# Kernel optimization log

Hardware: AMD Instinct MI355X
Metric: run time of the kernel (lower is better)

Reference implementation:

```python
import jax, jax.numpy as jnp
import numpy as np

# SSD-style extra-layer channel pyramid for sample_duration=16 (reconstructed):
CH = [(2048, 512, 1024), (1024, 256, 512), (512, 128, 256)]
DN = ('NCDHW', 'OIDHW', 'NCDHW')
B = 128


def conv3d(x, w, stride=(1, 1, 1), padding='VALID', rhs_dilation=None):
    return jax.lax.conv_general_dilated(
        x, w, window_strides=stride, padding=padding,
        rhs_dilation=rhs_dilation, dimension_numbers=DN)


def setup_inputs() -> dict:
    key = jax.random.key(0)
    ks = iter(jax.random.split(key, 32))
    s = 0.02
    d = {}
    d['x'] = jax.random.normal(next(ks), (B, 2048, 16, 2, 2), jnp.float32)
    d['start_boundaries'] = jax.random.randint(next(ks), (B,), 0, 1000, dtype=jnp.int32)
    # head 0 operates on the backbone feature map directly, kernel (2,2,2)
    d['loc_w0'] = s * jax.random.normal(next(ks), (2, 2048, 2, 2, 2), jnp.float32)
    d['conf_w0'] = s * jax.random.normal(next(ks), (3, 2048, 2, 2, 2), jnp.float32)
    for i, (cin, mid, cout) in enumerate(CH):
        d[f'e{i}_w1'] = s * jax.random.normal(next(ks), (mid, cin, 1, 1, 1), jnp.float32)
        d[f'e{i}_w2'] = s * jax.random.normal(next(ks), (cout, mid, 3, 3, 3), jnp.float32)
        d[f'loc_w{i+1}'] = s * jax.random.normal(next(ks), (2, cout, 2, 2, 2), jnp.float32)
        d[f'conf_w{i+1}'] = s * jax.random.normal(next(ks), (3, cout, 2, 2, 2), jnp.float32)
    return d


def reference(x, start_boundaries, loc_w0, conf_w0,
              e0_w1, e0_w2, loc_w1, conf_w1,
              e1_w1, e1_w2, loc_w2, conf_w2,
              e2_w1, e2_w2, loc_w3, conf_w3):
    del start_boundaries  # only used in test phase
    b = x.shape[0]
    loc_ws = [loc_w0, loc_w1, loc_w2, loc_w3]
    conf_ws = [conf_w0, conf_w1, conf_w2, conf_w3]
    extra = [(e0_w1, e0_w2), (e1_w1, e1_w2), (e2_w1, e2_w2)]
    locs = [conv3d(x, loc_ws[0]).reshape(b, -1)]
    confs = [conv3d(x, conf_ws[0]).reshape(b, -1)]
    h = x
    for i, (w1, w2) in enumerate(extra):
        h = conv3d(h, w1)  # 1x1x1 channel reduce
        # 3x3x3, temporal dilation/stride/padding 2 -> T halves, H/W preserved
        h = conv3d(h, w2, stride=(2, 1, 1),
                   padding=[(2, 2), (1, 1), (1, 1)], rhs_dilation=(2, 1, 1))
        locs.append(conv3d(h, loc_ws[i + 1]).reshape(b, -1))
        confs.append(conv3d(h, conf_ws[i + 1]).reshape(b, -1))
    loc = jnp.concatenate(locs, axis=1).reshape(b, -1, 2)    # [B, 26, 2]
    conf = jnp.concatenate(confs, axis=1).reshape(b, -1, 3)  # [B, 26, 3]
    return (loc, conf)
```

## Files before the change

kernel.cpp:

```cpp
#include <hip/hip_runtime.h>

typedef __bf16 bf16;
typedef bf16 bf16x2 __attribute__((ext_vector_type(2)));
typedef bf16 bf16x8 __attribute__((ext_vector_type(8)));
typedef float f32x4 __attribute__((ext_vector_type(4)));

__device__ __forceinline__ void gload16(const bf16* g, bf16* l) {
  __builtin_amdgcn_global_load_lds((const __attribute__((address_space(1))) void*)g,
                                   (__attribute__((address_space(3))) void*)l, 16, 0, 0);
}

template <bool FULL>
__global__ __launch_bounds__(256) void pack_x(const float* __restrict__ x, bf16* __restrict__ dstbuf) {
  __shared__ float tile[64 * 65];
  const int b = blockIdx.x, cb = blockIdx.y;
  const int t = threadIdx.x;
  const float* src = x + ((size_t)b * 2048 + cb * 64) * 64;
  #pragma unroll
  for (int p = 0; p < 16; ++p) {
    int idx = t + p * 256;
    tile[(idx >> 6) * 65 + (idx & 63)] = src[idx];
  }
  __syncthreads();
  if constexpr (FULL) {
    bf16* dst = dstbuf + (size_t)b * 131072 + cb * 64;
    #pragma unroll
    for (int p = 0; p < 8; ++p) {
      int idx = t + p * 256;
      int dhw = idx >> 5;
      int cl2 = (idx & 31) * 2;
      bf16x2 v;
      v.x = (bf16)tile[cl2 * 65 + dhw];
      v.y = (bf16)tile[(cl2 + 1) * 65 + dhw];
      *(bf16x2*)(dst + (size_t)dhw * 2048 + cl2) = v;
    }
  } else {
    bf16* dst = dstbuf + ((size_t)b * 32) * 2048 + cb * 64;
    const int cl2 = (t & 31) * 2, mr0 = t >> 5;
    #pragma unroll
    for (int p = 0; p < 4; ++p) {
      int mrow = mr0 + p * 8;
      int dd = mrow >> 2, hw = mrow & 3;
      int sdhw = dd * 8 + hw;
      bf16x2 v;
      v.x = (bf16)tile[cl2 * 65 + sdhw];
      v.y = (bf16)tile[(cl2 + 1) * 65 + sdhw];
      *(bf16x2*)(dst + (size_t)mrow * 2048 + cl2) = v;
    }
  }
}

__global__ __launch_bounds__(256) void pack_w0(const float* __restrict__ lw0,
                                               const float* __restrict__ cw0,
                                               bf16* __restrict__ Bh) {
  int idx = blockIdx.x * 256 + threadIdx.x;
  int n = idx >> 13, k = idx & 8191;
  int hw = k >> 11, c = k & 2047;
  float v = 0.f;
  if (n < 10) {
    int kd = n / 5, j = n % 5;
    const float* w = (j < 2) ? (lw0 + j * 16384) : (cw0 + (j - 2) * 16384);
    v = w[c * 8 + kd * 4 + hw];
  }
  Bh[idx] = (bf16)v;
}

__global__ __launch_bounds__(256) void head0_gemm(const bf16* __restrict__ xcl,
                                                  const bf16* __restrict__ Bh,
                                                  float* __restrict__ P) {
  __shared__ bf16 ldsA[64 * 64];
  __shared__ bf16 ldsB[16 * 64];
  const int bm = blockIdx.x, ks = blockIdx.y;
  const int tid = threadIdx.x;
  const int wv = tid >> 6, lane = tid & 63, r = lane & 15, g = lane >> 4;
  f32x4 acc = {0.f, 0.f, 0.f, 0.f};
  for (int k0 = 0; k0 < 1024; k0 += 64) {
    #pragma unroll
    for (int q = 0; q < 2; ++q) {
      int idx = tid + q * 256;
      int row = idx >> 3, cg = idx & 7;
      gload16(xcl + (size_t)(bm * 64 + row) * 8192 + ks * 1024 + k0 + (cg ^ (row & 7)) * 8,
              ldsA + idx * 8);
    }
    if (tid < 128) {
      int row = tid >> 3, cg = tid & 7;
      gload16(Bh + (size_t)row * 8192 + ks * 1024 + k0 + (cg ^ (row & 7)) * 8,
              ldsB + tid * 8);
    }
    __syncthreads();
    #pragma unroll
    for (int ks2 = 0; ks2 < 2; ++ks2) {
      int rowa = wv * 16 + r;
      bf16x8 af = *(const bf16x8*)(ldsA + rowa * 64 + ((ks2 * 4 + g) ^ (rowa & 7)) * 8);
      bf16x8 bf_ = *(const bf16x8*)(ldsB + r * 64 + ((ks2 * 4 + g) ^ (r & 7)) * 8);
      acc = __builtin_amdgcn_mfma_f32_16x16x32_bf16(af, bf_, acc, 0, 0, 0);
    }
    __syncthreads();
  }
  const int m = bm * 64 + wv * 16 + g * 4;
  #pragma unroll
  for (int jr = 0; jr < 4; ++jr)
    P[(size_t)(ks * 2048 + m + jr) * 16 + r] = acc[jr];
}

__global__ __launch_bounds__(128) void head0_combine(const float* __restrict__ P,
                                                     float* __restrict__ out) {
  const int b = blockIdx.x, t = threadIdx.x;
  if (t < 75) {
    int j = t / 15, d = t % 15;
    float s = 0.f;
    #pragma unroll
    for (int ks = 0; ks < 8; ++ks) {
      const float* pb = P + (size_t)(ks * 2048 + b * 16) * 16;
      s += pb[d * 16 + j] + pb[(d + 1) * 16 + 5 + j];
    }
    if (j < 2) out[b * 52 + j * 15 + d] = s;
    else       out[6656 + b * 78 + (j - 2) * 15 + d] = s;
  }
}

__global__ __launch_bounds__(256) void cvt_w1(const float* __restrict__ in, bf16* __restrict__ out, int n8) {
  int i = blockIdx.x * 256 + threadIdx.x;
  if (i < n8) {
    const float4* p = (const float4*)(in + (size_t)i * 8);
    float4 a = p[0], b = p[1];
    bf16x8 v = {(bf16)a.x, (bf16)a.y, (bf16)a.z, (bf16)a.w,
                (bf16)b.x, (bf16)b.y, (bf16)b.z, (bf16)b.w};
    *(bf16x8*)(out + (size_t)i * 8) = v;
  }
}

__global__ __launch_bounds__(256) void pack_w2(const float* __restrict__ w2, bf16* __restrict__ w2p,
                                               int oBase, int cin) {
  __shared__ float tile[64 * 27];
  const int orel = blockIdx.x, cb = blockIdx.y;
  const int o = oBase + orel;
  const float* src = w2 + ((size_t)o * cin + cb * 64) * 27;
  const int t = threadIdx.x;
  for (int idx = t; idx < 1728; idx += 256) tile[idx] = src[idx];
  __syncthreads();
  bf16* dst = w2p + (size_t)orel * 27 * cin + cb * 64;
  for (int idx = t; idx < 1728; idx += 256) {
    int tap = idx >> 6, cl = idx & 63;
    dst[(size_t)tap * cin + cl] = (bf16)tile[cl * 27 + tap];
  }
}

struct GP {
  const bf16* A; const bf16* B; bf16* O;
  int K;
  int ashb, asB, am1, as1, am2, as2;
  int oshb, osB, om1, os1, om2, os2, oOff;
  int lgCv, coutS, oCol0, lgCin;
};

template <int FM, int FN, bool W2M>
__global__ __launch_bounds__(256) void gemm_bf(GP p) {
  constexpr int BM = FM * 32, BN = FN * 32;
  __shared__ bf16 lds[(BM + BN) * 64];
  bf16* ldsA = lds;
  bf16* ldsB = lds + BM * 64;
  const int tid = threadIdx.x;
  const int bm = blockIdx.x, bn = blockIdx.y;

  int aBase[BM / 32], aL[BM / 32];
  #pragma unroll
  for (int q = 0; q < BM / 32; ++q) {
    int idx = tid + q * 256;
    int row = idx >> 3, cg = idx & 7;
    int m = bm * BM + row;
    aBase[q] = (m >> p.ashb) * p.asB + ((m >> 2) & p.am1) * p.as1 + (m & p.am2) * p.as2;
    aL[q] = ((cg ^ row) & 7) * 8;
  }
  int opk[BN / 32];
  int bN[BN / 32], bL[BN / 32];
  int khkw0 = 0, khkw1 = 0, khkw2 = 0, khkw3 = 0;
  #pragma unroll
  for (int q = 0; q < BN / 32; ++q) {
    int idx = tid + q * 256;
    int row = idx >> 3, cg = idx & 7;
    int n = bn * BN + row;
    int sw = ((cg ^ row) & 7) * 8;
    if constexpr (W2M) {
      int op = n & ((1 << p.lgCv) - 1);
      opk[q] = (op * 27 << p.lgCin) + sw;
      bN[q] = 0; bL[q] = 0;
    } else {
      bN[q] = n; bL[q] = sw; opk[q] = 0;
    }
  }
  if constexpr (W2M) {
    const int hwp = (bn * BN) >> p.lgCv;
    const int hp = hwp >> 1, wp = hwp & 1;
    khkw0 = ((1 - hp) * 3 + (1 - wp)) << p.lgCin;
    khkw1 = ((1 - hp) * 3 + (2 - wp)) << p.lgCin;
    khkw2 = ((2 - hp) * 3 + (1 - wp)) << p.lgCin;
    khkw3 = ((2 - hp) * 3 + (2 - wp)) << p.lgCin;
  }

  const int wv = tid >> 6, wm = wv >> 1, wn = wv & 1;
  const int lane = tid & 63, r = lane & 15, g = lane >> 4;

  f32x4 acc[FM][FN];
  const f32x4 zz = {0.f, 0.f, 0.f, 0.f};
  #pragma unroll
  for (int i = 0; i < FM; ++i)
    #pragma unroll
    for (int j = 0; j < FN; ++j) acc[i][j] = zz;

  for (int k0 = 0; k0 < p.K; k0 += 64) {
    #pragma unroll
    for (int q = 0; q < BM / 32; ++q) {
      int idx = tid + q * 256;
      gload16(p.A + aBase[q] + k0 + aL[q], ldsA + idx * 8);
    }
    if constexpr (W2M) {
      const int kd = k0 >> (p.lgCin + 2);
      const int hwsel = (k0 >> p.lgCin) & 3;
      const int c0 = k0 & ((1 << p.lgCin) - 1);
      int kk = (hwsel & 2) ? ((hwsel & 1) ? khkw3 : khkw2)
                           : ((hwsel & 1) ? khkw1 : khkw0);
      const int koff = (kd * 9 << p.lgCin) + kk + c0;
      #pragma unroll
      for (int q = 0; q < BN / 32; ++q) {
        int idx = tid + q * 256;
        gload16(p.B + opk[q] + koff, ldsB + idx * 8);
      }
    } else {
      #pragma unroll
      for (int q = 0; q < BN / 32; ++q) {
        int idx = tid + q * 256;
        gload16(p.B + (size_t)bN[q] * p.K + k0 + bL[q], ldsB + idx * 8);
      }
    }
    __syncthreads();
    #pragma unroll
    for (int ks = 0; ks < 2; ++ks) {
      bf16x8 af[FM], bfr[FN];
      #pragma unroll
      for (int i = 0; i < FM; ++i) {
        int row = wm * FM * 16 + i * 16 + r;
        int pcg = (ks * 4 + g) ^ (row & 7);
        af[i] = *(const bf16x8*)(ldsA + row * 64 + pcg * 8);
      }
      #pragma unroll
      for (int j = 0; j < FN; ++j) {
        int row = wn * FN * 16 + j * 16 + r;
        int pcg = (ks * 4 + g) ^ (row & 7);
        bfr[j] = *(const bf16x8*)(ldsB + row * 64 + pcg * 8);
      }
      #pragma unroll
      for (int i = 0; i < FM; ++i)
        #pragma unroll
        for (int j = 0; j < FN; ++j)
          acc[i][j] = __builtin_amdgcn_mfma_f32_16x16x32_bf16(af[i], bfr[j], acc[i][j], 0, 0, 0);
    }
    __syncthreads();
  }

  #pragma unroll
  for (int i = 0; i < FM; ++i) {
    #pragma unroll
    for (int j = 0; j < FN; ++j) {
      int ncol = bn * BN + wn * FN * 16 + j * 16 + r;
      int outcol = (ncol >> p.lgCv) * p.coutS + p.oCol0 + (ncol & ((1 << p.lgCv) - 1));
      #pragma unroll
      for (int jr = 0; jr < 4; ++jr) {
        int m = bm * BM + wm * FM * 16 + i * 16 + g * 4 + jr;
        int oa = (m >> p.oshb) * p.osB + ((m >> 2) & p.om1) * p.os1 + (m & p.om2) * p.os2 + p.oOff + outcol;
        p.O[oa] = (bf16)acc[i][j][jr];
      }
    }
  }
}

__global__ __launch_bounds__(256) void gemm2_sk64(const bf16* __restrict__ A,
                                                  const bf16* __restrict__ B,
                                                  float* __restrict__ Hf) {
  __shared__ bf16 lds[8192];
  bf16* ldsA = lds;
  bf16* ldsB = lds + 4096;
  const int tid = threadIdx.x;
  const int bm = blockIdx.x, bn = blockIdx.y, z = blockIdx.z;

  int aOff[2], bOff[2];
  #pragma unroll
  for (int q = 0; q < 2; ++q) {
    int idx = tid + q * 256;
    int row = idx >> 3, cg = idx & 7;
    int sw = ((cg ^ row) & 7) * 8;
    int m = bm * 64 + row;
    aOff[q] = (m >> 3) * 20480 + (m & 7) * 2048 + sw;
    int n = bn * 64 + row;
    bOff[q] = (n & 1023) * 13824 + sw;
  }
  const int hwp = (bn * 64) >> 10;
  const int hp = hwp >> 1, wp = hwp & 1;
  const int kk0 = ((1 - hp) * 3 + (1 - wp)) << 9;
  const int kk1 = ((1 - hp) * 3 + (2 - wp)) << 9;
  const int kk2 = ((2 - hp) * 3 + (1 - wp)) << 9;
  const int kk3 = ((2 - hp) * 3 + (2 - wp)) << 9;

  const int wv = tid >> 6, wm = wv >> 1, wn = wv & 1;
  const int lane = tid & 63, r = lane & 15, g = lane >> 4;

  f32x4 acc[2][2];
  const f32x4 zz = {0.f, 0.f, 0.f, 0.f};
  #pragma unroll
  for (int i = 0; i < 2; ++i)
    #pragma unroll
    for (int j = 0; j < 2; ++j) acc[i][j] = zz;

  const int kbeg = z * 3072, kend = kbeg + 3072;
  for (int k0 = kbeg; k0 < kend; k0 += 64) {
    int kd = k0 >> 11, hws = (k0 >> 9) & 3, c0 = k0 & 511;
    int kk = (hws & 2) ? ((hws & 1) ? kk3 : kk2) : ((hws & 1) ? kk1 : kk0);
    int koff = kd * 4608 + kk + c0;
    #pragma unroll
    for (int q = 0; q < 2; ++q) {
      int idx = tid + q * 256;
      gload16(A + aOff[q] + k0, ldsA + idx * 8);
      gload16(B + bOff[q] + koff, ldsB + idx * 8);
    }
    __syncthreads();
    #pragma unroll
    for (int ks = 0; ks < 2; ++ks) {
      bf16x8 af[2], bfr[2];
      #pragma unroll
      for (int i = 0; i < 2; ++i) {
        int row = wm * 32 + i * 16 + r;
        int pcg = (ks * 4 + g) ^ (row & 7);
        af[i] = *(const bf16x8*)(ldsA + row * 64 + pcg * 8);
      }
      #pragma unroll
      for (int j = 0; j < 2; ++j) {
        int row = wn * 32 + j * 16 + r;
        int pcg = (ks * 4 + g) ^ (row & 7);
        bfr[j] = *(const bf16x8*)(ldsB + row * 64 + pcg * 8);
      }
      #pragma unroll
      for (int i = 0; i < 2; ++i)
        #pragma unroll
        for (int j = 0; j < 2; ++j)
          acc[i][j] = __builtin_amdgcn_mfma_f32_16x16x32_bf16(af[i], bfr[j], acc[i][j], 0, 0, 0);
    }
    __syncthreads();
  }

  #pragma unroll
  for (int i = 0; i < 2; ++i) {
    #pragma unroll
    for (int j = 0; j < 2; ++j) {
      int col = bn * 64 + wn * 32 + j * 16 + r;
      #pragma unroll
      for (int jr = 0; jr < 4; ++jr) {
        int rw = bm * 64 + wm * 32 + i * 16 + g * 4 + jr;
        unsafeAtomicAdd(&Hf[(size_t)rw * 4096 + col], acc[i][j][jr]);
      }
    }
  }
}

__global__ __launch_bounds__(256) void cvt_h1b(const float* __restrict__ Hf,
                                               bf16* __restrict__ h1b) {
  size_t base = ((size_t)blockIdx.x * 256 + threadIdx.x) * 8;
  const float4* p = (const float4*)(Hf + base);
  float4 a = p[0], b = p[1];
  bf16x8 v = {(bf16)a.x, (bf16)a.y, (bf16)a.z, (bf16)a.w,
              (bf16)b.x, (bf16)b.y, (bf16)b.z, (bf16)b.w};
  *(bf16x8*)(h1b + base) = v;
}

template <typename T, bool XL>
__global__ __launch_bounds__(256)
void heads_k(const T* __restrict__ in, const float* __restrict__ wl,
             const float* __restrict__ wc, float* __restrict__ out,
             const int C, const int dcnt, const int sB, const int sD,
             const int sHW, const int sC, const int loff, const int coff) {
  const int tid = threadIdx.x;
  const int blk = blockIdx.x;
  const int b = blk / dcnt, d = blk - b * dcnt;
  float a0 = 0, a1 = 0, c0 = 0, c1 = 0, c2 = 0;
  const int C8 = C * 8;
  if constexpr (XL) {
    const int hw = tid & 3, kd = (tid >> 2) & 1, cb = tid >> 3;
    const int base = b * sB + (d + kd) * sD + hw * sHW;
    const int wb = kd * 4 + hw;
    for (int i = 0; i < C / 32; ++i) {
      const int c = cb + i * 32;
      const float v = (float)in[base + c * sC];
      const int wi = c * 8 + wb;
      a0 += v * wl[wi];  a1 += v * wl[C8 + wi];
      c0 += v * wc[wi];  c1 += v * wc[C8 + wi];  c2 += v * wc[2 * C8 + wi];
    }
  } else {
    for (int c = tid; c < C; c += 256) {
      #pragma unroll
      for (int kd = 0; kd < 2; ++kd) {
        #pragma unroll
        for (int hw = 0; hw < 4; ++hw) {
          const float v = (float)in[b * sB + (d + kd) * sD + hw * sHW + c];
          const int wi = c * 8 + kd * 4 + hw;
          a0 += v * wl[wi];  a1 += v * wl[C8 + wi];
          c0 += v * wc[wi];  c1 += v * wc[C8 + wi];  c2 += v * wc[2 * C8 + wi];
        }
      }
    }
  }
  #pragma unroll
  for (int off = 32; off; off >>= 1) {
    a0 += __shfl_down(a0, off, 64);
    a1 += __shfl_down(a1, off, 64);
    c0 += __shfl_down(c0, off, 64);
    c1 += __shfl_down(c1, off, 64);
    c2 += __shfl_down(c2, off, 64);
  }
  __shared__ float red[5][4];
  const int lane = tid & 63, wv = tid >> 6;
  if (lane == 0) { red[0][wv] = a0; red[1][wv] = a1; red[2][wv] = c0; red[3][wv] = c1; red[4][wv] = c2; }
  __syncthreads();
  if (tid == 0) {
    float L0 = red[0][0] + red[0][1] + red[0][2] + red[0][3];
    float L1 = red[1][0] + red[1][1] + red[1][2] + red[1][3];
    float F0 = red[2][0] + red[2][1] + red[2][2] + red[2][3];
    float F1 = red[3][0] + red[3][1] + red[3][2] + red[3][3];
    float F2 = red[4][0] + red[4][1] + red[4][2] + red[4][3];
    float* loc = out + (size_t)b * 52 + loff;
    loc[0 * dcnt + d] = L0;
    loc[1 * dcnt + d] = L1;
    float* cf = out + 6656 + (size_t)b * 78 + coff;
    cf[0 * dcnt + d] = F0;
    cf[1 * dcnt + d] = F1;
    cf[2 * dcnt + d] = F2;
  }
}

static void tail_layers(bf16* W, bf16* h1b, float* out,
                        const float* e1w1, const float* e1w2,
                        const float* lw2p, const float* cw2p,
                        const float* e2w1, const float* e2w2,
                        const float* lw3, const float* cw3,
                        const float* lw1, const float* cw1,
                        size_t W1c1, size_t h2a, size_t w2p1, size_t h2b,
                        size_t W1c2, size_t h3a, size_t w2p2, size_t h3b,
                        hipStream_t stream) {
  heads_k<bf16, false><<<128 * 7, 256, 0, stream>>>(
      h1b, lw1, cw1, out, 1024, 7, 32768, 4096, 1024, 1, 30, 45);
  hipMemsetAsync(W + h2a, 0, (size_t)786432 * 2, stream);
  cvt_w1<<<128, 256, 0, stream>>>(e1w1, W + W1c1, 32768);
  GP g3 = {h1b, W + W1c1, W + h2a, 1024,
           4, 32768, 3, 8192, 3, 1024,
           4, 6144, 3, 1024, 3, 256, 1024,
           8, 256, 0, 0};
  gemm_bf<1, 1, false><<<dim3(64, 8), 256, 0, stream>>>(g3);
  pack_w2<<<dim3(512, 4), 256, 0, stream>>>(e1w2, W + w2p1, 0, 256);
  GP g4 = {W + h2a, W + w2p1, W + h2b, 3072,
           2, 6144, 0, 0, 3, 1024,
           0, 2048, 0, 0, 0, 0, 0,
           9, 512, 0, 8};
  gemm_bf<1, 1, true><<<dim3(16, 64), 256, 0, stream>>>(g4);
  heads_k<bf16, false><<<128 * 3, 256, 0, stream>>>(
      W + h2b, lw2p, cw2p, out, 512, 3, 8192, 2048, 512, 1, 44, 66);

  hipMemsetAsync(W + h3a, 0, (size_t)262144 * 2, stream);
  cvt_w1<<<32, 256, 0, stream>>>(e2w1, W + W1c2, 8192);
  GP g5 = {W + h2b, W + W1c2, W + h3a, 512,
           3, 8192, 1, 4096, 3, 512,
           3, 2048, 1, 512, 3, 128, 512,
           7, 128, 0, 0};
  gemm_bf<1, 1, false><<<dim3(32, 4), 256, 0, stream>>>(g5);
  pack_w2<<<dim3(256, 2), 256, 0, stream>>>(e2w2, W + w2p2, 0, 128);
  GP g6 = {W + h3a, W + w2p2, W + h3b, 1536,
           1, 2048, 0, 0, 1, 512,
           0, 1024, 0, 0, 0, 0, 0,
           8, 256, 0, 7};
  gemm_bf<1, 1, true><<<dim3(8, 32), 256, 0, stream>>>(g6);
  heads_k<bf16, false><<<128 * 1, 256, 0, stream>>>(
      W + h3b, lw3, cw3, out, 256, 1, 2048, 1024, 256, 1, 50, 75);
}

extern "C" void kernel_launch(void* const* d_in, const int* in_sizes, int n_in,
                              void* d_out, int out_size, void* d_ws, size_t ws_size,
                              hipStream_t stream) {
  (void)in_sizes; (void)n_in; (void)out_size;
  const float* x    = (const float*)d_in[0];
  const float* lw0  = (const float*)d_in[2];
  const float* cw0  = (const float*)d_in[3];
  const float* e0w1 = (const float*)d_in[4];
  const float* e0w2 = (const float*)d_in[5];
  const float* lw1  = (const float*)d_in[6];
  const float* cw1  = (const float*)d_in[7];
  const float* e1w1 = (const float*)d_in[8];
  const float* e1w2 = (const float*)d_in[9];
  const float* lw2  = (const float*)d_in[10];
  const float* cw2  = (const float*)d_in[11];
  const float* e2w1 = (const float*)d_in[12];
  const float* e2w2 = (const float*)d_in[13];
  const float* lw3  = (const float*)d_in[14];
  const float* cw3  = (const float*)d_in[15];
  float* out = (float*)d_out;
  bf16* W = (bf16*)d_ws;

  if (ws_size >= (size_t)50400000) {
    const size_t xclo = 0;
    const size_t W1f  = 16777216;
    const size_t Bho  = 17825792;
    const size_t Po   = 17956864;
    const size_t h1ao = 22544384;
    const size_t w2p0 = 8388608;
    float* Hf = (float*)W;
    bf16* h1b = W + 8388608;

    hipMemsetAsync(W + h1ao, 0, (size_t)2621440 * 2, stream);
    pack_x<true><<<dim3(128, 32), 256, 0, stream>>>(x, W + xclo);
    pack_w0<<<512, 256, 0, stream>>>(lw0, cw0, W + Bho);
    head0_gemm<<<dim3(32, 8), 256, 0, stream>>>(W + xclo, W + Bho, (float*)(W + Po));
    head0_combine<<<128, 128, 0, stream>>>((float*)(W + Po), out);
    cvt_w1<<<512, 256, 0, stream>>>(e0w1, W + W1f, 131072);

    GP g1 = {W + xclo, W + W1f, W + h1ao, 2048,
             5, 131072, 7, 16384, 3, 2048,
             5, 20480, 7, 2048, 3, 512, 2048,
             9, 512, 0, 0};
    gemm_bf<2, 2, false><<<dim3(64, 8), 256, 0, stream>>>(g1);

    hipMemsetAsync(Hf, 0, (size_t)16777216, stream);
    pack_w2<<<dim3(1024, 8), 256, 0, stream>>>(e0w2, W + w2p0, 0, 512);
    gemm2_sk64<<<dim3(16, 64, 2), 256, 0, stream>>>(W + h1ao, W + w2p0, Hf);
    cvt_h1b<<<2048, 256, 0, stream>>>(Hf, h1b);

    tail_layers(W, h1b, out, e1w1, e1w2, lw2, cw2, e2w1, e2w2, lw3, cw3, lw1, cw1,
                0, 262144, 1048576, 4587520, 6684672, 6750208, 7012352, 7897088, stream);
    return;
  }

  if (ws_size >= (size_t)49283072) {
    const size_t xclo = 0;
    const size_t W1f  = 16777216;
    const size_t h1af = 17825792;
    const size_t h1bf = 20447232;
    const size_t w2p0f = 0;
    bf16* Bh = W + h1bf;
    float* P = (float*)(W + h1bf + 131072);

    hipMemsetAsync(W + h1af, 0, (size_t)2621440 * 2, stream);
    pack_x<true><<<dim3(128, 32), 256, 0, stream>>>(x, W + xclo);
    pack_w0<<<512, 256, 0, stream>>>(lw0, cw0, Bh);
    head0_gemm<<<dim3(32, 8), 256, 0, stream>>>(W + xclo, Bh, P);
    head0_combine<<<128, 128, 0, stream>>>(P, out);
    cvt_w1<<<512, 256, 0, stream>>>(e0w1, W + W1f, 131072);

    GP g1 = {W + xclo, W + W1f, W + h1af, 2048,
             5, 131072, 7, 16384, 3, 2048,
             5, 20480, 7, 2048, 3, 512, 2048,
             9, 512, 0, 0};
    gemm_bf<2, 2, false><<<dim3(64, 8), 256, 0, stream>>>(g1);

    pack_w2<<<dim3(1024, 8), 256, 0, stream>>>(e0w2, W + w2p0f, 0, 512);
    GP g2 = {W + h1af, W + w2p0f, W + h1bf, 6144,
             3, 20480, 0, 0, 7, 2048,
             0, 4096, 0, 0, 0, 0, 0,
             10, 1024, 0, 9};
    gemm_bf<2, 2, true><<<dim3(16, 64), 256, 0, stream>>>(g2);

    tail_layers(W, W + h1bf, out, e1w1, e1w2, lw2, cw2, e2w1, e2w2, lw3, cw3, lw1, cw1,
                0, 262144, 1048576, 4587520, 6684672, 6750208, 7012352, 7897088, stream);
    return;
  }

  const size_t A0o  = 0;
  const size_t W1o  = 8388608;
  const size_t h1ao = 9437184;
  const size_t h1bo = 12058624;
  const size_t W1c1 = 8388608, W1c2 = 8650752, h3ao = 8716288, h3bo = 8978432;
  const size_t h2ao = 9437184, h2bo = 12058624;
  const size_t w2p0o = 0, w2p1o = 0, w2p2o = 3538944;

  hipMemsetAsync(W + h1ao, 0, (size_t)2621440 * 2, stream);
  pack_x<false><<<dim3(128, 32), 256, 0, stream>>>(x, W + A0o);
  cvt_w1<<<512, 256, 0, stream>>>(e0w1, W + W1o, 131072);

  GP g1 = {W + A0o, W + W1o, W + h1ao, 2048,
           0, 2048, 0, 0, 0, 0,
           5, 20480, 7, 2048, 3, 512, 2048,
           9, 512, 0, 0};
  gemm_bf<2, 2, false><<<dim3(64, 8), 256, 0, stream>>>(g1);

  pack_w2<<<dim3(512, 8), 256, 0, stream>>>(e0w2, W + w2p0o, 0, 512);
  GP g2a = {W + h1ao, W + w2p0o, W + h1bo, 6144,
            3, 20480, 0, 0, 7, 2048,
            0, 4096, 0, 0, 0, 0, 0,
            9, 1024, 0, 9};
  gemm_bf<2, 2, true><<<dim3(16, 32), 256, 0, stream>>>(g2a);
  pack_w2<<<dim3(512, 8), 256, 0, stream>>>(e0w2, W + w2p0o, 512, 512);
  GP g2b = {W + h1ao, W + w2p0o, W + h1bo, 6144,
            3, 20480, 0, 0, 7, 2048,
            0, 4096, 0, 0, 0, 0, 0,
            9, 1024, 512, 9};
  gemm_bf<2, 2, true><<<dim3(16, 32), 256, 0, stream>>>(g2b);

  heads_k<bf16, false><<<128 * 7, 256, 0, stream>>>(
      W + h1bo, lw1, cw1, out, 1024, 7, 32768, 4096, 1024, 1, 30, 45);

  hipMemsetAsync(W + h2ao, 0, (size_t)786432 * 2, stream);
  cvt_w1<<<128, 256, 0, stream>>>(e1w1, W + W1c1, 32768);
  GP g3 = {W + h1bo, W + W1c1, W + h2ao, 1024,
           4, 32768, 3, 8192, 3, 1024,
           4, 6144, 3, 1024, 3, 256, 1024,
           8, 256, 0, 0};
  gemm_bf<1, 1, false><<<dim3(64, 8), 256, 0, stream>>>(g3);
  pack_w2<<<dim3(512, 4), 256, 0, stream>>>(e1w2, W + w2p1o, 0, 256);
  GP g4 = {W + h2ao, W + w2p1o, W + h2bo, 3072,
           2, 6144, 0, 0, 3, 1024,
           0, 2048, 0, 0, 0, 0, 0,
           9, 512, 0, 8};
  gemm_bf<1, 1, true><<<dim3(16, 64), 256, 0, stream>>>(g4);
  heads_k<bf16, false><<<128 * 3, 256, 0, stream>>>(
      W + h2bo, lw2, cw2, out, 512, 3, 8192, 2048, 512, 1, 44, 66);

  hipMemsetAsync(W + h3ao, 0, (size_t)262144 * 2, stream);
  cvt_w1<<<32, 256, 0, stream>>>(e2w1, W + W1c2, 8192);
  GP g5 = {W + h2bo, W + W1c2, W + h3ao, 512,
           3, 8192, 1, 4096, 3, 512,
           3, 2048, 1, 512, 3, 128, 512,
           7, 128, 0, 0};
  gemm_bf<1, 1, false><<<dim3(32, 4), 256, 0, stream>>>(g5);
  pack_w2<<<dim3(256, 2), 256, 0, stream>>>(e2w2, W + w2p2o, 0, 128);
  GP g6 = {W + h3ao, W + w2p2o, W + h3bo, 1536,
           1, 2048, 0, 0, 1, 512,
           0, 1024, 0, 0, 0, 0, 0,
           8, 256, 0, 7};
  gemm_bf<1, 1, true><<<dim3(8, 32), 256, 0, stream>>>(g6);
  heads_k<bf16, false><<<128 * 1, 256, 0, stream>>>(
      W + h3bo, lw3, cw3, out, 256, 1, 2048, 1024, 256, 1, 50, 75);

  heads_k<float, true><<<128 * 15, 256, 0, stream>>>(
      x, lw0, cw0, out, 2048, 15, 131072, 4, 1, 64, 0, 0);
}
```

Measured before the change: 270.6 us.

## Enlarge split-K tiles to 128x128 with XCD-aware block mapping for layer-0 3x3x3 GEMM

The split-K layer-0 3x3x3 conv GEMM now uses 128x128 tiles with a 4x4 MFMA fragment per wave, replacing 64x64 tiles. A flattened block index is remapped so blocks sharing B-column tiles land on the same XCD, which should improve L2 reuse. Larger tiles cut redundant A/B global traffic but raise register and LDS use and shrink the grid to 512 blocks. A second path gets a dedicated swizzled full-K kernel in place of the generic gemm_bf.

```diff
diff --git a/kernel.cpp b/kernel.cpp
--- a/kernel.cpp
+++ b/kernel.cpp
@@ -274,14 +274,118 @@
   }
 }
 
-__global__ __launch_bounds__(256) void gemm2_sk64(const bf16* __restrict__ A,
-                                                  const bf16* __restrict__ B,
-                                                  float* __restrict__ Hf) {
+__global__ __launch_bounds__(256) void gemm2_sk128(const bf16* __restrict__ A,
+                                                   const bf16* __restrict__ B,
+                                                   float* __restrict__ Hf) {
+  __shared__ bf16 lds[16384];
+  bf16* ldsA = lds;
+  bf16* ldsB = lds + 8192;
+  const int tid = threadIdx.x;
+  const int id = blockIdx.x;
+  const int xcd = id & 7, w = id >> 3;
+  const int bn = xcd * 4 + (w & 3);
+  const int bm = (w >> 2) & 7;
+  const int z  = w >> 5;
+
+  int aOff[4], bOff[4];
+  #pragma unroll
+  for (int q = 0; q < 4; ++q) {
+    int idx = tid + q * 256;
+    int row = idx >> 3, cg = idx & 7;
+    int sw = ((cg ^ row) & 7) * 8;
+    int m = bm * 128 + row;
+    aOff[q] = (m >> 3) * 20480 + (m & 7) * 2048 + sw;
+    int n = bn * 128 + row;
+    bOff[q] = (n & 1023) * 13824 + sw;
+  }
+  const int hwp = (bn * 128) >> 10;
+  const int hp = hwp >> 1, wp = hwp & 1;
+  const int kk0 = ((1 - hp) * 3 + (1 - wp)) << 9;
+  const int kk1 = ((1 - hp) * 3 + (2 - wp)) << 9;
+  const int kk2 = ((2 - hp) * 3 + (1 - wp)) << 9;
+  const int kk3 = ((2 - hp) * 3 + (2 - wp)) << 9;
+
+  const int wv = tid >> 6, wm = wv >> 1, wn = wv & 1;
+  const int lane = tid & 63, r = lane & 15, g = lane >> 4;
+
+  f32x4 acc[4][4];
+  const f32x4 zz = {0.f, 0.f, 0.f, 0.f};
+  #pragma unroll
+  for (int i = 0; i < 4; ++i)
+    #pragma unroll
+    for (int j = 0; j < 4; ++j) acc[i][j] = zz;
+
+  const int kbeg = z * 3072, kend = kbeg + 3072;
+  for (int k0 = kbeg; k0 < kend; k0 += 64) {
+    int kd = k0 >> 11, hws = (k0 >> 9) & 3, c0 = k0 & 511;
+    int kk = (hws & 2) ? ((hws & 1) ? kk3 : kk2) : ((hws & 1) ? kk1 : kk0);
+    int koff = kd * 4608 + kk + c0;
+    #pragma unroll
+    for (int q = 0; q < 4; ++q) {
+      int idx = tid + q * 256;
+      gload16(A + aOff[q] + k0, ldsA + idx * 8);
+      gload16(B + bOff[q] + koff, ldsB + idx * 8);
+    }
+    __syncthreads();
+    #pragma unroll
+    for (int ks = 0; ks < 2; ++ks) {
+      bf16x8 af[4], bfr[4];
+      #pragma unroll
+      for (int i = 0; i < 4; ++i) {
+        int row = wm * 64 + i * 16 + r;
+        int pcg = (ks * 4 + g) ^ (row & 7);
+        af[i] = *(const bf16x8*)(ldsA + row * 64 + pcg * 8);
+      }
+      #pragma unroll
+      for (int j = 0; j < 4; ++j) {
+        int row = wn * 64 + j * 16 + r;
+        int pcg = (ks * 4 + g) ^ (row & 7);
+        bfr[j] = *(const bf16x8*)(ldsB + row * 64 + pcg * 8);
+      }
+      #pragma unroll
+      for (int i = 0; i < 4; ++i)
+        #pragma unroll
+        for (int j = 0; j < 4; ++j)
+          acc[i][j] = __builtin_amdgcn_mfma_f32_16x16x32_bf16(af[i], bfr[j], acc[i][j], 0, 0, 0);
+    }
+    __syncthreads();
+  }
+
+  #pragma unroll
+  for (int i = 0; i < 4; ++i) {
+    #pragma unroll
+    for (int j = 0; j < 4; ++j) {
+      int col = bn * 128 + wn * 64 + j * 16 + r;
+      #pragma unroll
+      for (int jr = 0; jr < 4; ++jr) {
+        int rw = bm * 128 + wm * 64 + i * 16 + g * 4 + jr;
+        unsafeAtomicAdd(&Hf[(size_t)rw * 4096 + col], acc[i][j][jr]);
+      }
+    }
+  }
+}
+
+__global__ __launch_bounds__(256) void cvt_h1b(const float* __restrict__ Hf,
+                                               bf16* __restrict__ h1b) {
+  size_t base = ((size_t)blockIdx.x * 256 + threadIdx.x) * 8;
+  const float4* p = (const float4*)(Hf + base);
+  float4 a = p[0], b = p[1];
+  bf16x8 v = {(bf16)a.x, (bf16)a.y, (bf16)a.z, (bf16)a.w,
+              (bf16)b.x, (bf16)b.y, (bf16)b.z, (bf16)b.w};
+  *(bf16x8*)(h1b + base) = v;
+}
+
+__global__ __launch_bounds__(256) void gemm2_swz(const bf16* __restrict__ A,
+                                                 const bf16* __restrict__ B,
+                                                 bf16* __restrict__ O) {
   __shared__ bf16 lds[8192];
   bf16* ldsA = lds;
   bf16* ldsB = lds + 4096;
   const int tid = threadIdx.x;
-  const int bm = blockIdx.x, bn = blockIdx.y, z = blockIdx.z;
+  const int id = blockIdx.x + (blockIdx.y << 4);
+  const int s = id >> 3;
+  const int bn = (id & 7) * 8 + (s & 7);
+  const int bm = s >> 3;
 
   int aOff[2], bOff[2];
   #pragma unroll
@@ -311,8 +415,7 @@
     #pragma unroll
     for (int j = 0; j < 2; ++j) acc[i][j] = zz;
 
-  const int kbeg = z * 3072, kend = kbeg + 3072;
-  for (int k0 = kbeg; k0 < kend; k0 += 64) {
+  for (int k0 = 0; k0 < 6144; k0 += 64) {
     int kd = k0 >> 11, hws = (k0 >> 9) & 3, c0 = k0 & 511;
     int kk = (hws & 2) ? ((hws & 1) ? kk3 : kk2) : ((hws & 1) ? kk1 : kk0);
     int koff = kd * 4608 + kk + c0;
@@ -355,20 +458,10 @@
       #pragma unroll
       for (int jr = 0; jr < 4; ++jr) {
         int rw = bm * 64 + wm * 32 + i * 16 + g * 4 + jr;
-        unsafeAtomicAdd(&Hf[(size_t)rw * 4096 + col], acc[i][j][jr]);
-      }
-    }
-  }
-}
-
-__global__ __launch_bounds__(256) void cvt_h1b(const float* __restrict__ Hf,
-                                               bf16* __restrict__ h1b) {
-  size_t base = ((size_t)blockIdx.x * 256 + threadIdx.x) * 8;
-  const float4* p = (const float4*)(Hf + base);
-  float4 a = p[0], b = p[1];
-  bf16x8 v = {(bf16)a.x, (bf16)a.y, (bf16)a.z, (bf16)a.w,
-              (bf16)b.x, (bf16)b.y, (bf16)b.z, (bf16)b.w};
-  *(bf16x8*)(h1b + base) = v;
+        O[(size_t)rw * 4096 + col] = (bf16)acc[i][j][jr];
+      }
+    }
+  }
 }
 
 template <typename T, bool XL>
@@ -526,7 +619,7 @@
 
     hipMemsetAsync(Hf, 0, (size_t)16777216, stream);
     pack_w2<<<dim3(1024, 8), 256, 0, stream>>>(e0w2, W + w2p0, 0, 512);
-    gemm2_sk64<<<dim3(16, 64, 2), 256, 0, stream>>>(W + h1ao, W + w2p0, Hf);
+    gemm2_sk128<<<512, 256, 0, stream>>>(W + h1ao, W + w2p0, Hf);
     cvt_h1b<<<2048, 256, 0, stream>>>(Hf, h1b);
 
     tail_layers(W, h1b, out, e1w1, e1w2, lw2, cw2, e2w1, e2w2, lw3, cw3, lw1, cw1,
@@ -557,11 +650,7 @@
     gemm_bf<2, 2, false><<<dim3(64, 8), 256, 0, stream>>>(g1);
 
     pack_w2<<<dim3(1024, 8), 256, 0, stream>>>(e0w2, W + w2p0f, 0, 512);
-    GP g2 = {W + h1af, W + w2p0f, W + h1bf, 6144,
-             3, 20480, 0, 0, 7, 2048,
-             0, 4096, 0, 0, 0, 0, 0,
-             10, 1024, 0, 9};
-    gemm_bf<2, 2, true><<<dim3(16, 64), 256, 0, stream>>>(g2);
+    gemm2_swz<<<dim3(16, 64), 256, 0, stream>>>(W + h1af, W + w2p0f, W + h1bf);
 
     tail_layers(W, W + h1bf, out, e1w1, e1w2, lw2, cw2, e2w1, e2w2, lw3, cw3, lw1, cw1,
                 0, 262144, 1048576, 4587520, 6684672, 6750208, 7012352, 7897088, stream);
```

After: 261.3 us. 1.04x faster.
